# Optimization experiments

Hardware: AMD Instinct MI355X
Metric: run time of the kernel (lower is better)

Reference implementation:

```python
import jax, jax.numpy as jnp
import numpy as np

E = 256      # embedding_dim
H = 8        # num_heads
D = E // H   # head_dim = 32
F = 1024     # dim_feedforward
EPS = 1e-5


def layer_norm(x, gamma, beta):
    mu = jnp.mean(x, axis=-1, keepdims=True)
    var = jnp.var(x, axis=-1, keepdims=True)
    return (x - mu) * jax.lax.rsqrt(var + EPS) * gamma + beta


def setup_inputs() -> dict:
    key = jax.random.key(0)
    ks = jax.random.split(key, 12)
    s = lambda fan_in: 1.0 / np.sqrt(fan_in)
    src = jax.random.normal(ks[0], (4, 2048, E), dtype=jnp.float32)
    w_in = jax.random.uniform(ks[1], (3 * E, E), minval=-s(E), maxval=s(E), dtype=jnp.float32)
    w_out = jax.random.uniform(ks[2], (E, E), minval=-s(E), maxval=s(E), dtype=jnp.float32)
    w1 = jax.random.uniform(ks[3], (F, E), minval=-s(E), maxval=s(E), dtype=jnp.float32)
    b1 = jax.random.uniform(ks[4], (F,), minval=-s(E), maxval=s(E), dtype=jnp.float32)
    w2 = jax.random.uniform(ks[5], (E, F), minval=-s(F), maxval=s(F), dtype=jnp.float32)
    b2 = jax.random.uniform(ks[6], (E,), minval=-s(F), maxval=s(F), dtype=jnp.float32)
    g1 = jnp.ones((E,), jnp.float32)
    beta1 = jnp.zeros((E,), jnp.float32)
    g2 = jnp.ones((E,), jnp.float32)
    beta2 = jnp.zeros((E,), jnp.float32)
    return {"src": src, "w_in": w_in, "w_out": w_out, "w1": w1, "b1": b1,
            "w2": w2, "b2": b2, "g1": g1, "beta1": beta1, "g2": g2, "beta2": beta2}


def reference(src, w_in, w_out, w1, b1, w2, b2, g1, beta1, g2, beta2):
    B, S, _ = src.shape
    scale = D ** (-0.5)
    # --- pre-norm self-attention block ---
    x = layer_norm(src, g1, beta1)                 # [B,S,E]
    qkv = x @ w_in.T                               # [B,S,3E]
    q, k, v = jnp.split(qkv, 3, axis=-1)
    q = q.reshape(B, S, H, D).transpose(0, 2, 1, 3)  # [B,H,S,D]
    k = k.reshape(B, S, H, D).transpose(0, 2, 1, 3)
    v = v.reshape(B, S, H, D).transpose(0, 2, 1, 3)
    scores = jnp.einsum('bhqd,bhkd->bhqk', q, k) * scale  # [B,H,S,S]
    attn = jax.nn.softmax(scores, axis=-1)
    out = jnp.einsum('bhqk,bhkd->bhqd', attn, v)   # [B,H,S,D]
    out = out.transpose(0, 2, 1, 3).reshape(B, S, E)
    src = src + out @ w_out.T
    # --- pre-norm FFN block ---
    y = layer_norm(src, g2, beta2)
    y = jax.nn.relu(y @ w1.T + b1) @ w2.T + b2
    return src + y
```

## Files before the change

kernel.cpp:

```cpp
#include <hip/hip_runtime.h>
#include <hip/hip_bf16.h>
#include <math.h>

typedef unsigned short u16;
typedef unsigned int   u32;
using bf16x8 = __attribute__((ext_vector_type(8))) short;
using f32x4  = __attribute__((ext_vector_type(4))) float;
using f32x16 = __attribute__((ext_vector_type(16))) float;
using u32v4  = __attribute__((ext_vector_type(4))) u32;

#define TE 256
#define TH 8
#define TS 2048
#define TB 4
#define NTOK 8192
#define QSCALE 0.2550120651552454f
#define EXP2(x) __builtin_amdgcn_exp2f(x)

__device__ __forceinline__ void async16(const u16* g, u16* l) {
    __builtin_amdgcn_global_load_lds(
        (const __attribute__((address_space(1))) u32*)g,
        (__attribute__((address_space(3))) u32*)l, 16, 0, 0);
}
__device__ __forceinline__ u32 pkbf(float a, float b) {
    u32 ua = __float_as_uint(a) + 0x8000u;
    u32 ub = __float_as_uint(b) + 0x8000u;
    return __builtin_amdgcn_perm(ub, ua, 0x07060302u);
}
__device__ __forceinline__ u16 bf1(float a) {
    return (u16)((__float_as_uint(a) + 0x8000u) >> 16);
}

__device__ __forceinline__ void ln_body(const float* __restrict__ in,
        u16* __restrict__ out, const float* __restrict__ gamma,
        const float* __restrict__ beta, int rowblk) {
    int row  = rowblk * 4 + (threadIdx.x >> 6);
    int lane = threadIdx.x & 63;
    float4 v = ((const float4*)(in + (size_t)row * TE))[lane];
    float s  = v.x + v.y + v.z + v.w;
    float s2 = v.x*v.x + v.y*v.y + v.z*v.z + v.w*v.w;
    #pragma unroll
    for (int off = 32; off > 0; off >>= 1) {
        s  += __shfl_down(s,  off, 64);
        s2 += __shfl_down(s2, off, 64);
    }
    s  = __shfl(s,  0, 64);
    s2 = __shfl(s2, 0, 64);
    float mu = s * (1.f / TE);
    float rs = rsqrtf(s2 * (1.f / TE) - mu * mu + 1e-5f);
    float4 g = ((const float4*)gamma)[lane];
    float4 b = ((const float4*)beta )[lane];
    u32 lo = pkbf((v.x - mu) * rs * g.x + b.x, (v.y - mu) * rs * g.y + b.y);
    u32 hi = pkbf((v.z - mu) * rs * g.z + b.z, (v.w - mu) * rs * g.w + b.w);
    ((uint2*)(out + (size_t)row * TE))[lane] = make_uint2(lo, hi);
}

__global__ __launch_bounds__(256) void prep(const float* __restrict__ s0, u16* d0,
        const float* __restrict__ s1, u16* d1, const float* __restrict__ s2, u16* d2,
        const float* __restrict__ s3, u16* d3, const float* __restrict__ src,
        u16* __restrict__ xb, const float* __restrict__ g1,
        const float* __restrict__ be1) {
    if (blockIdx.x < 768) {
        int i = (blockIdx.x * 256 + threadIdx.x) * 4;
        const float* s; u16* d;
        if      (i < 196608) { s = s0; d = d0; }
        else if (i < 262144) { s = s1; d = d1; i -= 196608; }
        else if (i < 524288) { s = s2; d = d2; i -= 262144; }
        else                 { s = s3; d = d3; i -= 524288; }
        float4 v = *(const float4*)(s + i);
        *(uint2*)(d + i) = make_uint2(pkbf(v.x, v.y), pkbf(v.z, v.w));
    } else {
        ln_body(src, xb, g1, be1, blockIdx.x - 768);
    }
}

template<int K, int BM, int EPI>
__global__ __launch_bounds__(256) void mgemm(const u16* __restrict__ A,
        const u16* __restrict__ W, const float* __restrict__ bias,
        const float* __restrict__ R, float* __restrict__ Cf,
        u16* __restrict__ Cb, int M) {
    constexpr int BN = BM;
    __shared__ u16 Al[2][BM * 32];
    __shared__ u16 Wl[2][BN * 32];
    const int tid = threadIdx.x, w = tid >> 6, l = tid & 63;
    const int n0 = blockIdx.y * BM;
    const int m0 = blockIdx.x * BN;
    constexpr int NT = (BM == 128) ? 4 : 2;
    constexpr int NF = (BM == 128) ? 4 : 2;
    const int tw = (w & 1) * NT * 16;
    const int fw = (w >> 1) * NF * 16;
    const int fr = l & 15, fq = l >> 4;
    const int sr = l >> 2, sc = (l & 3) * 8;
    f32x4 acc[NT][NF];
    #pragma unroll
    for (int t = 0; t < NT; t++)
        #pragma unroll
        for (int f = 0; f < NF; f++)
            #pragma unroll
            for (int r = 0; r < 4; r++) acc[t][f][r] = 0.f;

    for (int k0 = 0; k0 < K; k0 += 64) {
        __syncthreads();
        #pragma unroll
        for (int hh = 0; hh < 2; hh++) {
            const int kc = k0 + hh * 32;
            if (BM == 128) {
                #pragma unroll
                for (int c = 0; c < 2; c++) {
                    int rr = (w * 2 + c) * 16 + sr;
                    async16(A + (size_t)(n0 + rr) * K + kc + sc, &Al[hh][(w * 2 + c) * 512]);
                    async16(W + (size_t)(m0 + rr) * K + kc + sc, &Wl[hh][(w * 2 + c) * 512]);
                }
            } else {
                int rr = w * 16 + sr;
                async16(A + (size_t)(n0 + rr) * K + kc + sc, &Al[hh][w * 512]);
                async16(W + (size_t)(m0 + rr) * K + kc + sc, &Wl[hh][w * 512]);
            }
        }
        __syncthreads();
        #pragma unroll
        for (int hh = 0; hh < 2; hh++) {
            bf16x8 af[NT], wf[NF];
            #pragma unroll
            for (int t = 0; t < NT; t++)
                af[t] = *(const bf16x8*)&Al[hh][(tw + t * 16 + fr) * 32 + fq * 8];
            #pragma unroll
            for (int f = 0; f < NF; f++)
                wf[f] = *(const bf16x8*)&Wl[hh][(fw + f * 16 + fr) * 32 + fq * 8];
            #pragma unroll
            for (int t = 0; t < NT; t++)
                #pragma unroll
                for (int f = 0; f < NF; f++)
                    acc[t][f] = __builtin_amdgcn_mfma_f32_16x16x32_bf16(
                        wf[f], af[t], acc[t][f], 0, 0, 0);
        }
    }
    #pragma unroll
    for (int t = 0; t < NT; t++) {
        const int tok = n0 + tw + t * 16 + fr;
        #pragma unroll
        for (int f = 0; f < NF; f++) {
            const int fb = m0 + fw + f * 16 + fq * 4;
            f32x4 v = acc[t][f];
            if (EPI == 0) {
                if (fb < 256) {
                    *(uint2*)(Cb + (size_t)tok * 256 + fb) = make_uint2(
                        pkbf(v[0]*QSCALE, v[1]*QSCALE), pkbf(v[2]*QSCALE, v[3]*QSCALE));
                } else if (fb < 512) {
                    const int hh = (fb - 256) >> 5, dd = (fb - 256) & 31;
                    const int bh = (tok >> 11) * 8 + hh;
                    const int kv = tok & 2047, tile = kv >> 5, lq = kv & 31;
                    const int fg = dd >> 4, hg = (dd >> 3) & 1, j = dd & 7;
                    u16* kp = (u16*)bias +
                        (((((size_t)bh * 64 + tile) * 2 + fg) * 2 + hg) * 32 + lq) * 8 + j;
                    *(uint2*)kp = make_uint2(pkbf(v[0], v[1]), pkbf(v[2], v[3]));
                } else {
                    const int hh = (fb - 512) >> 5, dd = (fb - 512) & 31;
                    const int bh = (tok >> 11) * 8 + hh;
                    const int kv = tok & 2047, tile = kv >> 5, kvr = kv & 31;
                    const int fg = kvr >> 4, hg = (kvr >> 3) & 1, j = kvr & 7;
                    u16* vp = (u16*)R +
                        ((((size_t)bh * 64 + tile) * 2 + fg) * 2 + hg) * 256 +
                        (size_t)dd * 8 + j;
                    vp[0]  = bf1(v[0]);
                    vp[8]  = bf1(v[1]);
                    vp[16] = bf1(v[2]);
                    vp[24] = bf1(v[3]);
                }
            } else if (EPI == 2) {
                float4 b4 = *(const float4*)(bias + fb);
                *(uint2*)(Cb + (size_t)tok * M + fb) = make_uint2(
                    pkbf(fmaxf(v[0]+b4.x, 0.f), fmaxf(v[1]+b4.y, 0.f)),
                    pkbf(fmaxf(v[2]+b4.z, 0.f), fmaxf(v[3]+b4.w, 0.f)));
            } else {
                float4 b4 = *(const float4*)(bias + fb);
                float4 r4 = *(const float4*)(R + (size_t)tok * M + fb);
                *(float4*)(Cf + (size_t)tok * M + fb) = make_float4(
                    v[0]+b4.x+r4.x, v[1]+b4.y+r4.y, v[2]+b4.z+r4.z, v[3]+b4.w+r4.w);
            }
        }
    }
}

__global__ __launch_bounds__(512) void g4ln(const u16* __restrict__ A,
        const u16* __restrict__ W, const float* __restrict__ src,
        float* __restrict__ out, u16* __restrict__ x2b,
        const float* __restrict__ g2, const float* __restrict__ be2) {
    __shared__ __align__(16) char smem[36864];
    u16* Al = (u16*)smem;
    u16* Wl = (u16*)(smem + 4096);
    const int tid = threadIdx.x, w = tid >> 6, l = tid & 63;
    const int tg = w & 1, fg = w >> 1;
    const int fr = l & 15, fq = l >> 4;
    const int sr = l >> 2, sc = (l & 3) * 8;
    const int n0 = blockIdx.x * 32;
    f32x4 acc[4];
    #pragma unroll
    for (int f = 0; f < 4; f++)
        #pragma unroll
        for (int r = 0; r < 4; r++) acc[f][r] = 0.f;

    auto stage = [&](int st, int buf) {
        const int kc = st * 32;
        const int rr = w * 16 + sr;
        async16(W + (size_t)rr * 256 + kc + sc, &Wl[buf * 8192 + w * 512]);
        async16(W + (size_t)(rr + 128) * 256 + kc + sc, &Wl[buf * 8192 + 4096 + w * 512]);
        if (w < 2) async16(A + (size_t)(n0 + rr) * 256 + kc + sc, &Al[buf * 1024 + w * 512]);
    };

    stage(0, 0);
    __syncthreads();
    #pragma unroll 2
    for (int st = 0; st < 8; ++st) {
        const int buf = st & 1;
        if (st + 1 < 8) stage(st + 1, buf ^ 1);
        bf16x8 af = *(const bf16x8*)&Al[buf * 1024 + (tg * 16 + fr) * 32 + fq * 8];
        bf16x8 wf[4];
        #pragma unroll
        for (int f = 0; f < 4; f++)
            wf[f] = *(const bf16x8*)&Wl[buf * 8192 + (fg * 64 + f * 16 + fr) * 32 + fq * 8];
        #pragma unroll
        for (int f = 0; f < 4; f++)
            acc[f] = __builtin_amdgcn_mfma_f32_16x16x32_bf16(wf[f], af, acc[f], 0, 0, 0);
        __syncthreads();
    }
    float* T = (float*)smem;
    const int tokl = tg * 16 + fr;
    const int tok  = n0 + tokl;
    #pragma unroll
    for (int f = 0; f < 4; ++f) {
        const int fb = fg * 64 + f * 16 + fq * 4;
        float4 s4 = *(const float4*)(src + (size_t)tok * 256 + fb);
        f32x4 v = acc[f];
        float4 o4 = make_float4(v[0]+s4.x, v[1]+s4.y, v[2]+s4.z, v[3]+s4.w);
        *(float4*)(out + (size_t)tok * 256 + fb) = o4;
        *(float4*)&T[tokl * 260 + fb] = o4;
    }
    __syncthreads();
    float4 gg = ((const float4*)g2)[l];
    float4 bb = ((const float4*)be2)[l];
    #pragma unroll
    for (int rr = 0; rr < 4; ++rr) {
        const int r = w * 4 + rr;
        float4 x = *(const float4*)&T[r * 260 + l * 4];
        float s  = x.x + x.y + x.z + x.w;
        float s2 = x.x*x.x + x.y*x.y + x.z*x.z + x.w*x.w;
        #pragma unroll
        for (int off = 32; off > 0; off >>= 1) {
            s  += __shfl_down(s,  off, 64);
            s2 += __shfl_down(s2, off, 64);
        }
        s  = __shfl(s,  0, 64);
        s2 = __shfl(s2, 0, 64);
        float mu = s * (1.f / 256.f);
        float rs = rsqrtf(s2 * (1.f / 256.f) - mu * mu + 1e-5f);
        u32 lo = pkbf((x.x - mu) * rs * gg.x + bb.x, (x.y - mu) * rs * gg.y + bb.y);
        u32 hi = pkbf((x.z - mu) * rs * gg.z + bb.z, (x.w - mu) * rs * gg.w + bb.w);
        *(uint2*)(x2b + (size_t)(n0 + r) * 256 + l * 4) = make_uint2(lo, hi);
    }
}

__global__ __launch_bounds__(256, 4) void attn_k(const u16* __restrict__ qb,
        const u16* __restrict__ kfb, const u16* __restrict__ vfb,
        u16* __restrict__ attn) {
    const int id = blockIdx.x;
    const int bh   = (id & 7) * 4 + (id >> 8);
    const int tile = (id >> 3) & 31;
    const int b = bh >> 3, h = bh & 7;
    const int tid = threadIdx.x, w = tid >> 6, l = tid & 63;
    const int qw = w & 1, kw = w >> 1;
    const int lq = l & 31, hi = l >> 5;
    const size_t btok = (size_t)b * TS;
    const int q0 = tile * 64 + qw * 32;

    __shared__ float mrg[2304];

    const u16* qrow = qb + (btok + q0 + lq) * 256 + h * 32 + hi * 8;
    bf16x8 qf0 = *(const bf16x8*)qrow;
    bf16x8 qf1 = *(const bf16x8*)(qrow + 16);

    f32x16 zf, o;
    #pragma unroll
    for (int r = 0; r < 16; r++) { zf[r] = 0.f; o[r] = 0.f; }
    float ps = 0.f;

    const u16* kp = kfb + ((size_t)bh * 64 + kw * 32) * 1024 + l * 8;
    const u16* vp = vfb + ((size_t)bh * 64 + kw * 32) * 1024 + l * 8;
    bf16x8 k0 = *(const bf16x8*)kp;
    bf16x8 k1 = *(const bf16x8*)(kp + 512);
    bf16x8 v0 = *(const bf16x8*)vp;
    bf16x8 v1 = *(const bf16x8*)(vp + 512);

    #pragma unroll 2
    for (int it = 0; it < 32; ++it) {
        kp += 1024; vp += 1024;
        bf16x8 nk0 = *(const bf16x8*)kp;
        bf16x8 nk1 = *(const bf16x8*)(kp + 512);
        bf16x8 nv0 = *(const bf16x8*)vp;
        bf16x8 nv1 = *(const bf16x8*)(vp + 512);
        f32x16 p = __builtin_amdgcn_mfma_f32_32x32x16_bf16(k0, qf0, zf, 0, 0, 0);
        p = __builtin_amdgcn_mfma_f32_32x32x16_bf16(k1, qf1, p, 0, 0, 0);
        float e[16];
        #pragma unroll
        for (int r = 0; r < 16; r++) e[r] = EXP2(p[r]);
        ps += ((e[0]+e[1]) + (e[2]+e[3])) + ((e[4]+e[5]) + (e[6]+e[7]))
            + ((e[8]+e[9]) + (e[10]+e[11])) + ((e[12]+e[13]) + (e[14]+e[15]));
        u32 a[8];
        #pragma unroll
        for (int j = 0; j < 8; j++)
            asm("v_cvt_pk_bf16_f32 %0, %1, %2"
                : "=v"(a[j]) : "v"(e[2*j]), "v"(e[2*j+1]));
        asm("v_permlane32_swap_b32 %0, %1" : "+v"(a[0]), "+v"(a[2]));
        asm("v_permlane32_swap_b32 %0, %1" : "+v"(a[1]), "+v"(a[3]));
        asm("v_permlane32_swap_b32 %0, %1" : "+v"(a[4]), "+v"(a[6]));
        asm("v_permlane32_swap_b32 %0, %1" : "+v"(a[5]), "+v"(a[7]));
        u32v4 t0 = {a[0], a[1], a[2], a[3]};
        u32v4 t1 = {a[4], a[5], a[6], a[7]};
        bf16x8 pf0 = __builtin_bit_cast(bf16x8, t0);
        bf16x8 pf1 = __builtin_bit_cast(bf16x8, t1);
        o = __builtin_amdgcn_mfma_f32_32x32x16_bf16(v0, pf0, o, 0, 0, 0);
        o = __builtin_amdgcn_mfma_f32_32x32x16_bf16(v1, pf1, o, 0, 0, 0);
        k0 = nk0; k1 = nk1; v0 = nv0; v1 = nv1;
    }
    ps += __shfl_xor(ps, 32, 64);

    if (kw == 1) {
        float* d = mrg + (qw * 64 + l) * 18;
        #pragma unroll
        for (int r = 0; r < 16; r++) d[r] = o[r];
        d[16] = ps;
    }
    __syncthreads();
    if (kw == 0) {
        const float* d = mrg + (qw * 64 + l) * 18;
        #pragma unroll
        for (int r = 0; r < 16; r++) o[r] += d[r];
        ps += d[16];
        float inv = 1.f / ps;
        int tok = (int)btok + q0 + lq;
        u16* orow = attn + (size_t)tok * 256 + h * 32 + hi * 4;
        #pragma unroll
        for (int g = 0; g < 4; g++)
            *(uint2*)(orow + g * 8) = make_uint2(
                pkbf(o[4*g]*inv, o[4*g+1]*inv), pkbf(o[4*g+2]*inv, o[4*g+3]*inv));
    }
}

extern "C" void kernel_launch(void* const* d_in, const int* in_sizes, int n_in,
                              void* d_out, int out_size, void* d_ws, size_t ws_size,
                              hipStream_t stream) {
    const float* src  = (const float*)d_in[0];
    const float* w_in = (const float*)d_in[1];
    const float* w_out= (const float*)d_in[2];
    const float* w1   = (const float*)d_in[3];
    const float* b1   = (const float*)d_in[4];
    const float* w2   = (const float*)d_in[5];
    const float* b2   = (const float*)d_in[6];
    const float* g1   = (const float*)d_in[7];
    const float* be1  = (const float*)d_in[8];
    const float* g2   = (const float*)d_in[9];
    const float* be2  = (const float*)d_in[10];
    float* out = (float*)d_out;

    u16* xb    = (u16*)d_ws;
    u16* qb    = xb + (size_t)NTOK * 256;
    u16* kfbuf = qb + (size_t)NTOK * 256;
    u16* vfbuf = kfbuf + (size_t)32 * 64 * 1024;
    u16* attnb = xb;
    u16* h1b   = (u16*)d_ws;
    u16* x2b   = (u16*)((char*)d_ws + (size_t)NTOK * 1024 * 2);
    u16* wib   = x2b + (size_t)NTOK * 256;
    u16* wob   = wib + 768 * 256;
    u16* w1b   = wob + 256 * 256;
    u16* w2b   = w1b + 1024 * 256;

    prep<<<768 + NTOK / 4, 256, 0, stream>>>(
        w_in, wib, w_out, wob, w1, w1b, w2, w2b, src, xb, g1, be1);
    mgemm<256, 128, 0><<<dim3(6, 64), 256, 0, stream>>>(
        xb, wib, (const float*)kfbuf, (const float*)vfbuf, nullptr, qb, 768);
    attn_k<<<dim3(1024), 256, 0, stream>>>(qb, kfbuf, vfbuf, attnb);
    g4ln<<<256, 512, 0, stream>>>(attnb, wob, src, out, x2b, g2, be2);
    mgemm<256, 128, 2><<<dim3(8, 64), 256, 0, stream>>>(
        x2b, w1b, b1, nullptr, nullptr, h1b, 1024);
    mgemm<1024, 64, 3><<<dim3(4, 128), 256, 0, stream>>>(
        h1b, w2b, b2, out, out, nullptr, 256);
}
```

Before: 159.6 us.

## Split attention keys four ways per block, each wave handling both query halves

Before, each of the four waves handled one 32-query half and one key half. Now every wave processes all 64 queries of the tile as two 32-row groups, and the keys are split four ways, 16 chunks per wave. Each K/V fragment loaded is therefore reused across two query groups, halving per-wave K/V global loads and making two independent MFMA chains available to overlap. In exchange the wave holds two accumulators and two sets of exp/convert temporaries, which raises register pressure, and the final merge becomes a three-way LDS reduction done by a single wave.

```diff
diff --git a/kernel.cpp b/kernel.cpp
--- a/kernel.cpp
+++ b/kernel.cpp
@@ -268,81 +268,108 @@
     const int tile = (id >> 3) & 31;
     const int b = bh >> 3, h = bh & 7;
     const int tid = threadIdx.x, w = tid >> 6, l = tid & 63;
-    const int qw = w & 1, kw = w >> 1;
     const int lq = l & 31, hi = l >> 5;
     const size_t btok = (size_t)b * TS;
-    const int q0 = tile * 64 + qw * 32;
-
-    __shared__ float mrg[2304];
-
-    const u16* qrow = qb + (btok + q0 + lq) * 256 + h * 32 + hi * 8;
-    bf16x8 qf0 = *(const bf16x8*)qrow;
-    bf16x8 qf1 = *(const bf16x8*)(qrow + 16);
-
-    f32x16 zf, o;
-    #pragma unroll
-    for (int r = 0; r < 16; r++) { zf[r] = 0.f; o[r] = 0.f; }
-    float ps = 0.f;
-
-    const u16* kp = kfb + ((size_t)bh * 64 + kw * 32) * 1024 + l * 8;
-    const u16* vp = vfb + ((size_t)bh * 64 + kw * 32) * 1024 + l * 8;
+    const int q0 = tile * 64;
+
+    __shared__ float mrg[3 * 64 * 35];
+
+    const u16* qrowA = qb + (btok + q0 + lq) * 256 + h * 32 + hi * 8;
+    bf16x8 qf0a = *(const bf16x8*)qrowA;
+    bf16x8 qf1a = *(const bf16x8*)(qrowA + 16);
+    const u16* qrowB = qrowA + 32 * 256;
+    bf16x8 qf0b = *(const bf16x8*)qrowB;
+    bf16x8 qf1b = *(const bf16x8*)(qrowB + 16);
+
+    f32x16 zf, oa, ob;
+    #pragma unroll
+    for (int r = 0; r < 16; r++) { zf[r] = 0.f; oa[r] = 0.f; ob[r] = 0.f; }
+    float psA = 0.f, psB = 0.f;
+
+    const u16* kp = kfb + ((size_t)bh * 64 + w * 16) * 1024 + l * 8;
+    const u16* vp = vfb + ((size_t)bh * 64 + w * 16) * 1024 + l * 8;
     bf16x8 k0 = *(const bf16x8*)kp;
     bf16x8 k1 = *(const bf16x8*)(kp + 512);
     bf16x8 v0 = *(const bf16x8*)vp;
     bf16x8 v1 = *(const bf16x8*)(vp + 512);
 
     #pragma unroll 2
-    for (int it = 0; it < 32; ++it) {
+    for (int it = 0; it < 16; ++it) {
         kp += 1024; vp += 1024;
         bf16x8 nk0 = *(const bf16x8*)kp;
         bf16x8 nk1 = *(const bf16x8*)(kp + 512);
         bf16x8 nv0 = *(const bf16x8*)vp;
         bf16x8 nv1 = *(const bf16x8*)(vp + 512);
-        f32x16 p = __builtin_amdgcn_mfma_f32_32x32x16_bf16(k0, qf0, zf, 0, 0, 0);
-        p = __builtin_amdgcn_mfma_f32_32x32x16_bf16(k1, qf1, p, 0, 0, 0);
-        float e[16];
-        #pragma unroll
-        for (int r = 0; r < 16; r++) e[r] = EXP2(p[r]);
-        ps += ((e[0]+e[1]) + (e[2]+e[3])) + ((e[4]+e[5]) + (e[6]+e[7]))
-            + ((e[8]+e[9]) + (e[10]+e[11])) + ((e[12]+e[13]) + (e[14]+e[15]));
-        u32 a[8];
-        #pragma unroll
-        for (int j = 0; j < 8; j++)
+        f32x16 pA = __builtin_amdgcn_mfma_f32_32x32x16_bf16(k0, qf0a, zf, 0, 0, 0);
+        f32x16 pB = __builtin_amdgcn_mfma_f32_32x32x16_bf16(k0, qf0b, zf, 0, 0, 0);
+        pA = __builtin_amdgcn_mfma_f32_32x32x16_bf16(k1, qf1a, pA, 0, 0, 0);
+        pB = __builtin_amdgcn_mfma_f32_32x32x16_bf16(k1, qf1b, pB, 0, 0, 0);
+        float eA[16], eB[16];
+        #pragma unroll
+        for (int r = 0; r < 16; r++) { eA[r] = EXP2(pA[r]); eB[r] = EXP2(pB[r]); }
+        psA += ((eA[0]+eA[1]) + (eA[2]+eA[3])) + ((eA[4]+eA[5]) + (eA[6]+eA[7]))
+             + ((eA[8]+eA[9]) + (eA[10]+eA[11])) + ((eA[12]+eA[13]) + (eA[14]+eA[15]));
+        psB += ((eB[0]+eB[1]) + (eB[2]+eB[3])) + ((eB[4]+eB[5]) + (eB[6]+eB[7]))
+             + ((eB[8]+eB[9]) + (eB[10]+eB[11])) + ((eB[12]+eB[13]) + (eB[14]+eB[15]));
+        u32 aA[8], aB[8];
+        #pragma unroll
+        for (int j = 0; j < 8; j++) {
             asm("v_cvt_pk_bf16_f32 %0, %1, %2"
-                : "=v"(a[j]) : "v"(e[2*j]), "v"(e[2*j+1]));
-        asm("v_permlane32_swap_b32 %0, %1" : "+v"(a[0]), "+v"(a[2]));
-        asm("v_permlane32_swap_b32 %0, %1" : "+v"(a[1]), "+v"(a[3]));
-        asm("v_permlane32_swap_b32 %0, %1" : "+v"(a[4]), "+v"(a[6]));
-        asm("v_permlane32_swap_b32 %0, %1" : "+v"(a[5]), "+v"(a[7]));
-        u32v4 t0 = {a[0], a[1], a[2], a[3]};
-        u32v4 t1 = {a[4], a[5], a[6], a[7]};
-        bf16x8 pf0 = __builtin_bit_cast(bf16x8, t0);
-        bf16x8 pf1 = __builtin_bit_cast(bf16x8, t1);
-        o = __builtin_amdgcn_mfma_f32_32x32x16_bf16(v0, pf0, o, 0, 0, 0);
-        o = __builtin_amdgcn_mfma_f32_32x32x16_bf16(v1, pf1, o, 0, 0, 0);
+                : "=v"(aA[j]) : "v"(eA[2*j]), "v"(eA[2*j+1]));
+            asm("v_cvt_pk_bf16_f32 %0, %1, %2"
+                : "=v"(aB[j]) : "v"(eB[2*j]), "v"(eB[2*j+1]));
+        }
+        asm("v_permlane32_swap_b32 %0, %1" : "+v"(aA[0]), "+v"(aA[2]));
+        asm("v_permlane32_swap_b32 %0, %1" : "+v"(aA[1]), "+v"(aA[3]));
+        asm("v_permlane32_swap_b32 %0, %1" : "+v"(aA[4]), "+v"(aA[6]));
+        asm("v_permlane32_swap_b32 %0, %1" : "+v"(aA[5]), "+v"(aA[7]));
+        asm("v_permlane32_swap_b32 %0, %1" : "+v"(aB[0]), "+v"(aB[2]));
+        asm("v_permlane32_swap_b32 %0, %1" : "+v"(aB[1]), "+v"(aB[3]));
+        asm("v_permlane32_swap_b32 %0, %1" : "+v"(aB[4]), "+v"(aB[6]));
+        asm("v_permlane32_swap_b32 %0, %1" : "+v"(aB[5]), "+v"(aB[7]));
+        u32v4 tA0 = {aA[0], aA[1], aA[2], aA[3]};
+        u32v4 tA1 = {aA[4], aA[5], aA[6], aA[7]};
+        u32v4 tB0 = {aB[0], aB[1], aB[2], aB[3]};
+        u32v4 tB1 = {aB[4], aB[5], aB[6], aB[7]};
+        bf16x8 pfA0 = __builtin_bit_cast(bf16x8, tA0);
+        bf16x8 pfA1 = __builtin_bit_cast(bf16x8, tA1);
+        bf16x8 pfB0 = __builtin_bit_cast(bf16x8, tB0);
+        bf16x8 pfB1 = __builtin_bit_cast(bf16x8, tB1);
+        oa = __builtin_amdgcn_mfma_f32_32x32x16_bf16(v0, pfA0, oa, 0, 0, 0);
+        ob = __builtin_amdgcn_mfma_f32_32x32x16_bf16(v0, pfB0, ob, 0, 0, 0);
+        oa = __builtin_amdgcn_mfma_f32_32x32x16_bf16(v1, pfA1, oa, 0, 0, 0);
+        ob = __builtin_amdgcn_mfma_f32_32x32x16_bf16(v1, pfB1, ob, 0, 0, 0);
         k0 = nk0; k1 = nk1; v0 = nv0; v1 = nv1;
     }
-    ps += __shfl_xor(ps, 32, 64);
-
-    if (kw == 1) {
-        float* d = mrg + (qw * 64 + l) * 18;
-        #pragma unroll
-        for (int r = 0; r < 16; r++) d[r] = o[r];
-        d[16] = ps;
+    psA += __shfl_xor(psA, 32, 64);
+    psB += __shfl_xor(psB, 32, 64);
+
+    if (w > 0) {
+        float* d = mrg + ((w - 1) * 64 + l) * 35;
+        #pragma unroll
+        for (int r = 0; r < 16; r++) { d[r] = oa[r]; d[16 + r] = ob[r]; }
+        d[32] = psA; d[33] = psB;
     }
     __syncthreads();
-    if (kw == 0) {
-        const float* d = mrg + (qw * 64 + l) * 18;
-        #pragma unroll
-        for (int r = 0; r < 16; r++) o[r] += d[r];
-        ps += d[16];
-        float inv = 1.f / ps;
-        int tok = (int)btok + q0 + lq;
-        u16* orow = attn + (size_t)tok * 256 + h * 32 + hi * 4;
-        #pragma unroll
-        for (int g = 0; g < 4; g++)
-            *(uint2*)(orow + g * 8) = make_uint2(
-                pkbf(o[4*g]*inv, o[4*g+1]*inv), pkbf(o[4*g+2]*inv, o[4*g+3]*inv));
+    if (w == 0) {
+        #pragma unroll
+        for (int part = 0; part < 3; part++) {
+            const float* d = mrg + (part * 64 + l) * 35;
+            #pragma unroll
+            for (int r = 0; r < 16; r++) { oa[r] += d[r]; ob[r] += d[16 + r]; }
+            psA += d[32]; psB += d[33];
+        }
+        float invA = 1.f / psA, invB = 1.f / psB;
+        int tokA = (int)btok + q0 + lq;
+        u16* orowA = attn + (size_t)tokA * 256 + h * 32 + hi * 4;
+        u16* orowB = orowA + 32 * 256;
+        #pragma unroll
+        for (int g = 0; g < 4; g++) {
+            *(uint2*)(orowA + g * 8) = make_uint2(
+                pkbf(oa[4*g]*invA, oa[4*g+1]*invA), pkbf(oa[4*g+2]*invA, oa[4*g+3]*invA));
+            *(uint2*)(orowB + g * 8) = make_uint2(
+                pkbf(ob[4*g]*invB, ob[4*g+1]*invB), pkbf(ob[4*g+2]*invB, ob[4*g+3]*invB));
+        }
     }
 }
 
```

New measurement: 162.4 us. No clear change (+1.8%).
